# Optimization experiments

Measured on AMD Instinct MI355X. Metric: run time of the kernel, lower is better.

## Reference

```python
import jax, jax.numpy as jnp
import numpy as np

D_MODEL = 1024
NUM_HEADS = 16
HEAD_DIM = D_MODEL // NUM_HEADS
D_FF = 4096
BATCH = 4
SEQ = 2048
LN_EPS = 1e-6
NEG_INF = -1e10


def setup_inputs() -> dict:
    key = jax.random.key(0)
    ks = jax.random.split(key, 8)
    def lin_init(k, fan_in, fan_out):
        # flax default: lecun_normal kernel, zeros bias
        w = jax.random.normal(k, (fan_in, fan_out), jnp.float32) / np.sqrt(fan_in)
        b = jnp.zeros((fan_out,), jnp.float32)
        return w, b
    x = jax.random.normal(ks[0], (BATCH, SEQ, D_MODEL), jnp.float32)
    w_qkv, b_qkv = lin_init(ks[1], D_MODEL, 3 * D_MODEL)
    w_out, b_out = lin_init(ks[2], D_MODEL, D_MODEL)
    w_fc1, b_fc1 = lin_init(ks[3], D_MODEL, D_FF)
    w_fc2, b_fc2 = lin_init(ks[4], D_FF, D_MODEL)
    ln1_scale = jnp.ones((D_MODEL,), jnp.float32)
    ln1_bias = jnp.zeros((D_MODEL,), jnp.float32)
    ln2_scale = jnp.ones((D_MODEL,), jnp.float32)
    ln2_bias = jnp.zeros((D_MODEL,), jnp.float32)
    return {
        'x': x,
        'w_qkv': w_qkv, 'b_qkv': b_qkv,
        'w_out': w_out, 'b_out': b_out,
        'w_fc1': w_fc1, 'b_fc1': b_fc1,
        'w_fc2': w_fc2, 'b_fc2': b_fc2,
        'ln1_scale': ln1_scale, 'ln1_bias': ln1_bias,
        'ln2_scale': ln2_scale, 'ln2_bias': ln2_bias,
    }


def _layernorm(x, scale, bias):
    mu = jnp.mean(x, axis=-1, keepdims=True)
    var = jnp.mean(jnp.square(x - mu), axis=-1, keepdims=True)
    return (x - mu) * jax.lax.rsqrt(var + LN_EPS) * scale + bias


def _attention(x, w_qkv, b_qkv, w_out, b_out):
    B, S, _ = x.shape
    qkv = x @ w_qkv + b_qkv                      # [B,S,3*D]
    qkv = qkv.reshape(B, S, 3, NUM_HEADS, HEAD_DIM)
    q, k, v = qkv[:, :, 0], qkv[:, :, 1], qkv[:, :, 2]   # [B,S,H,D]
    q = q.transpose(0, 2, 1, 3)                  # [B,H,S,D]
    k = k.transpose(0, 2, 1, 3)
    v = v.transpose(0, 2, 1, 3)
    scores = jnp.einsum('bhqd,bhkd->bhqk', q, k) / np.sqrt(HEAD_DIM)
    causal = jnp.tril(jnp.ones((S, S), bool))[None, None]
    scores = jnp.where(causal, scores, NEG_INF)
    attn = jax.nn.softmax(scores, axis=-1)
    out = jnp.einsum('bhqk,bhkd->bhqd', attn, v)  # [B,H,S,D]
    out = out.transpose(0, 2, 1, 3).reshape(B, S, D_MODEL)
    return out @ w_out + b_out


def _mlp(x, w_fc1, b_fc1, w_fc2, b_fc2):
    h = jax.nn.gelu(x @ w_fc1 + b_fc1)  # approximate (tanh) gelu, matching nnx.gelu default
    return h @ w_fc2 + b_fc2


def reference(x, w_qkv, b_qkv, w_out, b_out, w_fc1, b_fc1, w_fc2, b_fc2,
              ln1_scale, ln1_bias, ln2_scale, ln2_bias):
    x = x + _attention(_layernorm(x, ln1_scale, ln1_bias), w_qkv, b_qkv, w_out, b_out)
    x = x + _mlp(_layernorm(x, ln2_scale, ln2_bias), w_fc1, b_fc1, w_fc2, b_fc2)
    return x
```

## Files before the change

kernel.cpp:

```cpp
#include <hip/hip_runtime.h>

typedef unsigned short u16;
typedef unsigned int u32;
typedef __bf16 bf16x8 __attribute__((ext_vector_type(8)));
typedef float f32x4 __attribute__((ext_vector_type(4)));

constexpr int SEQ = 2048;

__device__ __forceinline__ float bf2f(u16 u) {
    u32 x = ((u32)u) << 16;
    return __builtin_bit_cast(float, x);
}
__device__ __forceinline__ u16 f2bf(float f) {
    u32 u = __builtin_bit_cast(u32, f);
    u32 r = u + 0x7fffu + ((u >> 16) & 1u);
    return (u16)(r >> 16);
}
__device__ __forceinline__ u32 cvt_pk_bf16(float a, float b) {
    u32 d;
    asm("v_cvt_pk_bf16_f32 %0, %1, %2" : "=v"(d) : "v"(a), "v"(b));
    return d;
}
__device__ __forceinline__ bf16x8 ld_frag(const u16* p) {
    uint4 u = *(const uint4*)p;
    return __builtin_bit_cast(bf16x8, u);
}
__device__ __forceinline__ float gelu_f(float x) {
    float u = 0.7978845608028654f * (x + 0.044715f * x * x * x);
    float e = exp2f(u * 2.885390081777927f);
    float t = 1.f - 2.f / (1.f + e);
    return 0.5f * x * (1.f + t);
}
__device__ __forceinline__ bool probe_f32(const u32* p) { return (p[0] & 0xFFFFu) == 0u; }

__device__ __forceinline__ void load_lds16(const u16* g, u16* l) {
    __builtin_amdgcn_global_load_lds(
        (const __attribute__((address_space(1))) void*)g,
        (__attribute__((address_space(3))) void*)l, 16, 0, 0);
}

__device__ __forceinline__ void xcd_map(int& bx, int& by) {
    const int gx = gridDim.x;
    const int n = gx * gridDim.y;
    const int orig = blockIdx.y * gx + blockIdx.x;
    const int id = (orig & 7) * (n >> 3) + (orig >> 3);
    bx = id % gx;
    by = id / gx;
}

__global__ __launch_bounds__(256) void convert_to_bf16(const void* __restrict__ in, long long off,
                                                       u16* __restrict__ out, int n,
                                                       const u32* __restrict__ probe) {
    const bool f32 = probe_f32(probe);
    int i = (blockIdx.x * 256 + threadIdx.x) * 4;
    if (i >= n) return;
    if (f32) {
        const float4 v = *(const float4*)((const float*)in + off + i);
        uint2 o;
        o.x = (u32)f2bf(v.x) | ((u32)f2bf(v.y) << 16);
        o.y = (u32)f2bf(v.z) | ((u32)f2bf(v.w) << 16);
        *(uint2*)(out + i) = o;
    } else {
        *(uint2*)(out + i) = *(const uint2*)((const u16*)in + off + i);
    }
}

__global__ __launch_bounds__(256) void transpose_any(const void* __restrict__ in,
                                                     u16* __restrict__ out,
                                                     int K, int N, const u32* __restrict__ probe) {
    const bool f32 = probe_f32(probe);
    __shared__ u16 tile[32][33];
    int tx = threadIdx.x & 31, ty = threadIdx.x >> 5;
    int k0 = blockIdx.y * 32, n0 = blockIdx.x * 32;
    for (int i = 0; i < 32; i += 8) {
        size_t idx = (size_t)(k0 + ty + i) * N + n0 + tx;
        tile[ty + i][tx] = f32 ? f2bf(((const float*)in)[idx]) : ((const u16*)in)[idx];
    }
    __syncthreads();
    for (int i = 0; i < 32; i += 8)
        out[(size_t)(n0 + ty + i) * K + k0 + tx] = tile[tx][ty + i];
}

__global__ __launch_bounds__(256) void fused_cvt_ln(const void* __restrict__ xraw, long long off,
                                                    const u16* __restrict__ sc,
                                                    const u16* __restrict__ bi,
                                                    u16* __restrict__ xbf,
                                                    u16* __restrict__ xn,
                                                    const u32* __restrict__ probe) {
    const bool f32 = probe_f32(probe);
    int row = blockIdx.x;
    int tid = threadIdx.x;
    float v[4];
    if (f32) {
        const float4 q = *(const float4*)((const float*)xraw + off + (size_t)row * 1024 + tid * 4);
        v[0] = q.x; v[1] = q.y; v[2] = q.z; v[3] = q.w;
    } else {
        uint2 u = *(const uint2*)((const u16*)xraw + off + (size_t)row * 1024 + tid * 4);
        v[0] = bf2f((u16)(u.x & 0xffffu)); v[1] = bf2f((u16)(u.x >> 16));
        v[2] = bf2f((u16)(u.y & 0xffffu)); v[3] = bf2f((u16)(u.y >> 16));
    }
    {
        uint2 c;
        c.x = (u32)f2bf(v[0]) | ((u32)f2bf(v[1]) << 16);
        c.y = (u32)f2bf(v[2]) | ((u32)f2bf(v[3]) << 16);
        *(uint2*)(xbf + (size_t)row * 1024 + tid * 4) = c;
    }
    float s1 = 0.f, s2 = 0.f;
    for (int i = 0; i < 4; i++) { s1 += v[i]; s2 += v[i] * v[i]; }
    for (int off2 = 32; off2 >= 1; off2 >>= 1) {
        s1 += __shfl_xor(s1, off2, 64);
        s2 += __shfl_xor(s2, off2, 64);
    }
    __shared__ float red[8];
    int wave = tid >> 6, lane = tid & 63;
    if (lane == 0) { red[wave] = s1; red[4 + wave] = s2; }
    __syncthreads();
    s1 = red[0] + red[1] + red[2] + red[3];
    s2 = red[4] + red[5] + red[6] + red[7];
    float mean = s1 * (1.f / 1024.f);
    float var = s2 * (1.f / 1024.f) - mean * mean;
    float rstd = rsqrtf(var + 1e-6f);
    int c = tid * 4;
    float y0 = (v[0] - mean) * rstd * bf2f(sc[c + 0]) + bf2f(bi[c + 0]);
    float y1 = (v[1] - mean) * rstd * bf2f(sc[c + 1]) + bf2f(bi[c + 1]);
    float y2 = (v[2] - mean) * rstd * bf2f(sc[c + 2]) + bf2f(bi[c + 2]);
    float y3 = (v[3] - mean) * rstd * bf2f(sc[c + 3]) + bf2f(bi[c + 3]);
    uint2 ov;
    ov.x = (u32)f2bf(y0) | ((u32)f2bf(y1) << 16);
    ov.y = (u32)f2bf(y2) | ((u32)f2bf(y3) << 16);
    *(uint2*)(xn + (size_t)row * 1024 + tid * 4) = ov;
}

__global__ __launch_bounds__(256) void layernorm_k(const u16* __restrict__ x,
                                                   const u16* __restrict__ sc,
                                                   const u16* __restrict__ bi,
                                                   u16* __restrict__ out) {
    int row = blockIdx.x;
    int tid = threadIdx.x;
    const u16* xr = x + (size_t)row * 1024;
    uint2 u = *(const uint2*)(xr + tid * 4);
    float v[4];
    v[0] = bf2f((u16)(u.x & 0xffffu));
    v[1] = bf2f((u16)(u.x >> 16));
    v[2] = bf2f((u16)(u.y & 0xffffu));
    v[3] = bf2f((u16)(u.y >> 16));
    float s1 = 0.f, s2 = 0.f;
    for (int i = 0; i < 4; i++) { s1 += v[i]; s2 += v[i] * v[i]; }
    for (int off = 32; off >= 1; off >>= 1) {
        s1 += __shfl_xor(s1, off, 64);
        s2 += __shfl_xor(s2, off, 64);
    }
    __shared__ float red[8];
    int wave = tid >> 6, lane = tid & 63;
    if (lane == 0) { red[wave] = s1; red[4 + wave] = s2; }
    __syncthreads();
    s1 = red[0] + red[1] + red[2] + red[3];
    s2 = red[4] + red[5] + red[6] + red[7];
    float mean = s1 * (1.f / 1024.f);
    float var = s2 * (1.f / 1024.f) - mean * mean;
    float rstd = rsqrtf(var + 1e-6f);
    u32 o0, o1;
    {
        int c = tid * 4;
        float y0 = (v[0] - mean) * rstd * bf2f(sc[c + 0]) + bf2f(bi[c + 0]);
        float y1 = (v[1] - mean) * rstd * bf2f(sc[c + 1]) + bf2f(bi[c + 1]);
        float y2 = (v[2] - mean) * rstd * bf2f(sc[c + 2]) + bf2f(bi[c + 2]);
        float y3 = (v[3] - mean) * rstd * bf2f(sc[c + 3]) + bf2f(bi[c + 3]);
        o0 = (u32)f2bf(y0) | ((u32)f2bf(y1) << 16);
        o1 = (u32)f2bf(y2) | ((u32)f2bf(y3) << 16);
    }
    uint2 ov; ov.x = o0; ov.y = o1;
    *(uint2*)(out + (size_t)row * 1024 + tid * 4) = ov;
}

__device__ __forceinline__ void gemm_core(const u16* __restrict__ A, const u16* __restrict__ Bt,
                                          int K, int bm, int bn,
                                          u16* lA, u16* lB, f32x4 acc[4][4]) {
    const int tid = threadIdx.x, lane = tid & 63, wave = tid >> 6;
    const int wr = (wave >> 1) * 64, wc = (wave & 1) * 64;
    const int g = lane >> 4, l15 = lane & 15;
    const int srow = wave * 32 + (lane >> 3);
    const int gslot = (lane & 7) ^ (lane >> 3);
    const u16* gA = A + (size_t)(bm + srow) * K + gslot * 8;
    const u16* gB = Bt + (size_t)(bn + srow) * K + gslot * 8;
    const int sw = (l15 & 7);
    const int nt = K >> 6;

    {
        u16* dA = lA + wave * 2048;
        u16* dB = lB + wave * 2048;
#pragma unroll
        for (int q = 0; q < 4; q++) {
            load_lds16(gA + q * 8 * K, dA + q * 512);
            load_lds16(gB + q * 8 * K, dB + q * 512);
        }
    }

    for (int t = 0; t < nt; t++) {
        const int cur = (t & 1) * 8192;
        __syncthreads();
        if (t + 1 < nt) {
            const int nxt = ((t + 1) & 1) * 8192;
            const int kk = (t + 1) * 64;
            u16* dA = lA + nxt + wave * 2048;
            u16* dB = lB + nxt + wave * 2048;
#pragma unroll
            for (int q = 0; q < 4; q++) {
                load_lds16(gA + kk + q * 8 * K, dA + q * 512);
                load_lds16(gB + kk + q * 8 * K, dB + q * 512);
            }
        }
        const u16* cA = lA + cur;
        const u16* cB = lB + cur;
#pragma unroll
        for (int kh = 0; kh < 2; kh++) {
            bf16x8 af[4], bfr[4];
#pragma unroll
            for (int i = 0; i < 4; i++)
                af[i] = ld_frag(cA + (wr + i * 16 + l15) * 64 + (((kh * 4 + g) ^ sw) * 8));
#pragma unroll
            for (int j = 0; j < 4; j++)
                bfr[j] = ld_frag(cB + (wc + j * 16 + l15) * 64 + (((kh * 4 + g) ^ sw) * 8));
#pragma unroll
            for (int i = 0; i < 4; i++)
#pragma unroll
                for (int j = 0; j < 4; j++)
                    acc[i][j] = __builtin_amdgcn_mfma_f32_16x16x32_bf16(bfr[j], af[i], acc[i][j], 0, 0, 0);
        }
    }
}

__global__ __launch_bounds__(256) void gemm_bt(const u16* __restrict__ A,
                                               const u16* __restrict__ Bt,
                                               const u16* __restrict__ bias,
                                               const u16* __restrict__ res,
                                               void* __restrict__ out,
                                               int M, int N, int K, int epi,
                                               long long ooff, const u32* __restrict__ probe) {
    __shared__ __align__(16) u16 lA[2 * 128 * 64];
    __shared__ __align__(16) u16 lB[2 * 128 * 64];
    const int tid = threadIdx.x, lane = tid & 63, wave = tid >> 6;
    const int wr = (wave >> 1) * 64, wc = (wave & 1) * 64;
    const int g = lane >> 4, l15 = lane & 15;
    const int bm = blockIdx.y * 128, bn = blockIdx.x * 128;

    f32x4 acc[4][4];
    f32x4 zero = {0.f, 0.f, 0.f, 0.f};
    for (int i = 0; i < 4; i++)
        for (int j = 0; j < 4; j++) acc[i][j] = zero;

    gemm_core(A, Bt, K, bm, bn, lA, lB, acc);

    const bool of32 = (epi == 3) && probe_f32(probe);
    for (int j = 0; j < 4; j++) {
        const int gn0 = bn + wc + j * 16 + g * 4;
        const uint2 bv2 = *(const uint2*)(bias + gn0);
        const float b0 = bf2f((u16)(bv2.x & 0xffffu)), b1 = bf2f((u16)(bv2.x >> 16));
        const float b2 = bf2f((u16)(bv2.y & 0xffffu)), b3 = bf2f((u16)(bv2.y >> 16));
        for (int i = 0; i < 4; i++) {
            const int gm = bm + wr + i * 16 + l15;
            float v0 = acc[i][j][0] + b0, v1 = acc[i][j][1] + b1;
            float v2 = acc[i][j][2] + b2, v3 = acc[i][j][3] + b3;
            if (epi == 1 || epi == 3) {
                const uint2 rv = *(const uint2*)(res + (size_t)gm * N + gn0);
                v0 += bf2f((u16)(rv.x & 0xffffu)); v1 += bf2f((u16)(rv.x >> 16));
                v2 += bf2f((u16)(rv.y & 0xffffu)); v3 += bf2f((u16)(rv.y >> 16));
            } else if (epi == 2) {
                v0 = gelu_f(v0); v1 = gelu_f(v1); v2 = gelu_f(v2); v3 = gelu_f(v3);
            }
            if (epi == 3) {
                if (of32) {
                    float4 o = {v0, v1, v2, v3};
                    *(float4*)((float*)out + ooff + (size_t)gm * N + gn0) = o;
                } else {
                    uint2 o;
                    o.x = cvt_pk_bf16(v0, v1); o.y = cvt_pk_bf16(v2, v3);
                    *(uint2*)((u16*)out + ooff + (size_t)gm * N + gn0) = o;
                }
            } else {
                uint2 o;
                o.x = cvt_pk_bf16(v0, v1); o.y = cvt_pk_bf16(v2, v3);
                *(uint2*)((u16*)out + (size_t)gm * N + gn0) = o;
            }
        }
    }
}

__global__ __launch_bounds__(256) void gemm_qkv(const u16* __restrict__ A,
                                                const u16* __restrict__ Bt,
                                                const u16* __restrict__ bias,
                                                u16* __restrict__ Qg,
                                                u16* __restrict__ Kg,
                                                u16* __restrict__ VTg,
                                                int K) {
    __shared__ __align__(16) u16 lA[2 * 128 * 64];
    __shared__ __align__(16) u16 lB[2 * 128 * 64];
    const int tid = threadIdx.x, lane = tid & 63, wave = tid >> 6;
    const int wr = (wave >> 1) * 64, wc = (wave & 1) * 64;
    const int g = lane >> 4, l15 = lane & 15;
    const int bm = blockIdx.y * 128, bn = blockIdx.x * 128;
    const float QSCALE = 0.18033688011112042f;

    f32x4 acc[4][4];
    f32x4 zero = {0.f, 0.f, 0.f, 0.f};
    for (int i = 0; i < 4; i++)
        for (int j = 0; j < 4; j++) acc[i][j] = zero;

    gemm_core(A, Bt, K, bm, bn, lA, lB, acc);

    for (int j = 0; j < 4; j++) {
        const int gn0 = bn + wc + j * 16 + g * 4;
        const int which = gn0 >> 10;
        const int hh = (gn0 >> 6) & 15, d0 = gn0 & 63;
        const uint2 bv2 = *(const uint2*)(bias + gn0);
        const float b0 = bf2f((u16)(bv2.x & 0xffffu)), b1 = bf2f((u16)(bv2.x >> 16));
        const float b2 = bf2f((u16)(bv2.y & 0xffffu)), b3 = bf2f((u16)(bv2.y >> 16));
        for (int i = 0; i < 4; i++) {
            const int s0 = bm + wr + i * 16 + l15;
            const int b = s0 >> 11, srel = s0 & 2047;
            const int bh = b * 16 + hh;
            const float v0 = acc[i][j][0] + b0, v1 = acc[i][j][1] + b1;
            const float v2 = acc[i][j][2] + b2, v3 = acc[i][j][3] + b3;
            if (which == 0) {
                uint2 o;
                o.x = cvt_pk_bf16(v0 * QSCALE, v1 * QSCALE);
                o.y = cvt_pk_bf16(v2 * QSCALE, v3 * QSCALE);
                *(uint2*)(Qg + ((size_t)bh * SEQ + srel) * 64 + d0) = o;
            } else if (which == 1) {
                uint2 o;
                o.x = cvt_pk_bf16(v0, v1); o.y = cvt_pk_bf16(v2, v3);
                *(uint2*)(Kg + ((size_t)bh * SEQ + srel) * 64 + d0) = o;
            } else {
                VTg[((size_t)bh * 64 + d0 + 0) * SEQ + srel] = f2bf(v0);
                VTg[((size_t)bh * 64 + d0 + 1) * SEQ + srel] = f2bf(v1);
                VTg[((size_t)bh * 64 + d0 + 2) * SEQ + srel] = f2bf(v2);
                VTg[((size_t)bh * 64 + d0 + 3) * SEQ + srel] = f2bf(v3);
            }
        }
    }
}

__device__ __forceinline__ void stage_kv(const u16* Kbh, const u16* Vbh, int kv0,
                                         u16* bK, u16* bV, int lane, int wave) {
    const int r = lane >> 3;
    const int gs = ((lane & 7) ^ r) * 8;
#pragma unroll
    for (int q = 0; q < 2; q++) {
        const int row = q * 32 + wave * 8 + r;
        load_lds16(Kbh + (size_t)(kv0 + row) * 64 + gs, bK + q * 2048 + wave * 512 + lane * 8);
        load_lds16(Vbh + (size_t)row * SEQ + kv0 + gs, bV + q * 2048 + wave * 512 + lane * 8);
    }
}

__global__ __launch_bounds__(256) void flash_attn6(const u16* __restrict__ Qg,
                                                   const u16* __restrict__ Kg,
                                                   const u16* __restrict__ VTg,
                                                   u16* __restrict__ attn) {
    __shared__ __align__(16) u16 lK[2][64 * 64];
    __shared__ __align__(16) u16 lVt[2][64 * 64];
    __shared__ __align__(16) u16 lP[4 * 32 * 72];

    int bxi, byi;
    xcd_map(bxi, byi);
    const int bh = byi;
    const int tid = threadIdx.x, lane = tid & 63, wave = tid >> 6;
    const int g = lane >> 4, l15 = lane & 15;
    const float MASKV = -3.0e4f;

    const u16* Qbh = Qg + (size_t)bh * SEQ * 64;
    const u16* Kbh = Kg + (size_t)bh * SEQ * 64;
    const u16* Vbh = VTg + (size_t)bh * 64 * SEQ;
    u16* myP = lP + wave * 32 * 72;
    const int b = bh >> 4, h = bh & 15;
    const f32x4 zero = {0.f, 0.f, 0.f, 0.f};
    const int sw = (l15 & 7);

    for (int ph = 0; ph < 2; ph++) {
        const int ti = ph ? bxi : (15 - bxi);
        const int q0 = ti * 128;
        const int qw = q0 + wave * 32;
        const int nfull = q0 >> 6;
        const int nt = nfull + 2;

        bf16x8 qf[2][2];
#pragma unroll
        for (int mi = 0; mi < 2; mi++)
#pragma unroll
            for (int kh = 0; kh < 2; kh++)
                qf[mi][kh] = ld_frag(Qbh + (size_t)(qw + mi * 16 + l15) * 64 + kh * 32 + g * 8);

        float l_[2] = {0.f, 0.f};
        f32x4 o[2][4];
        for (int mi = 0; mi < 2; mi++)
            for (int nj = 0; nj < 4; nj++) o[mi][nj] = zero;

        __syncthreads();
        stage_kv(Kbh, Vbh, 0, lK[0], lVt[0], lane, wave);

        for (int t = 0; t < nt; t++) {
            __syncthreads();
            if (t + 1 < nt)
                stage_kv(Kbh, Vbh, (t + 1) * 64, lK[(t + 1) & 1], lVt[(t + 1) & 1], lane, wave);
            const u16* bK = lK[t & 1];
            const u16* bV = lVt[t & 1];
            const bool diag = (t >= nfull);
            const int kv0 = t * 64;

            f32x4 sc[4][2];
#pragma unroll
            for (int ki = 0; ki < 4; ki++)
                for (int mi = 0; mi < 2; mi++) sc[ki][mi] = zero;
#pragma unroll
            for (int kh = 0; kh < 2; kh++) {
                bf16x8 kf[4];
#pragma unroll
                for (int ki = 0; ki < 4; ki++)
                    kf[ki] = ld_frag(bK + (ki * 16 + l15) * 64 + (((kh * 4 + g) ^ sw) * 8));
#pragma unroll
                for (int ki = 0; ki < 4; ki++)
#pragma unroll
                    for (int mi = 0; mi < 2; mi++)
                        sc[ki][mi] = __builtin_amdgcn_mfma_f32_16x16x32_bf16(kf[ki], qf[mi][kh], sc[ki][mi], 0, 0, 0);
            }

#pragma unroll
            for (int mi = 0; mi < 2; mi++) {
                const int qrow = qw + mi * 16 + l15;
                u16* pr = myP + (mi * 16 + l15) * 72 + g * 4;
                float lacc = 0.f;
#pragma unroll
                for (int ki = 0; ki < 4; ki++) {
                    const int kvb = kv0 + ki * 16 + g * 4;
                    float v0 = sc[ki][mi][0], v1 = sc[ki][mi][1];
                    float v2 = sc[ki][mi][2], v3 = sc[ki][mi][3];
                    if (diag) {
                        if (kvb + 0 > qrow) v0 = MASKV;
                        if (kvb + 1 > qrow) v1 = MASKV;
                        if (kvb + 2 > qrow) v2 = MASKV;
                        if (kvb + 3 > qrow) v3 = MASKV;
                    }
                    const float e0 = exp2f(v0), e1 = exp2f(v1);
                    const float e2 = exp2f(v2), e3 = exp2f(v3);
                    lacc += (e0 + e1) + (e2 + e3);
                    uint2 pw;
                    pw.x = cvt_pk_bf16(e0, e1);
                    pw.y = cvt_pk_bf16(e2, e3);
                    *(uint2*)(pr + ki * 16) = pw;
                }
                l_[mi] += lacc;
            }

#pragma unroll
            for (int ks = 0; ks < 2; ks++) {
                bf16x8 pa[2], vb[4];
#pragma unroll
                for (int mi = 0; mi < 2; mi++)
                    pa[mi] = ld_frag(myP + (mi * 16 + l15) * 72 + ks * 32 + g * 8);
#pragma unroll
                for (int nj = 0; nj < 4; nj++)
                    vb[nj] = ld_frag(bV + (nj * 16 + l15) * 64 + (((ks * 4 + g) ^ sw) * 8));
#pragma unroll
                for (int mi = 0; mi < 2; mi++)
#pragma unroll
                    for (int nj = 0; nj < 4; nj++)
                        o[mi][nj] = __builtin_amdgcn_mfma_f32_16x16x32_bf16(pa[mi], vb[nj], o[mi][nj], 0, 0, 0);
            }
        }

#pragma unroll
        for (int mi = 0; mi < 2; mi++) {
            float ls = l_[mi];
            ls += __shfl_xor(ls, 16, 64);
            ls += __shfl_xor(ls, 32, 64);
#pragma unroll
            for (int r = 0; r < 4; r++) {
                const float inv = 1.f / __shfl(ls, g * 4 + r, 64);
                const int row = qw + mi * 16 + g * 4 + r;
                const size_t orow = ((size_t)b * SEQ + row) * 1024 + h * 64;
                for (int nj = 0; nj < 4; nj++)
                    attn[orow + nj * 16 + l15] = f2bf(o[mi][nj][r] * inv);
            }
        }
    }
}

extern "C" void kernel_launch(void* const* d_in, const int* in_sizes, int n_in,
                              void* d_out, int out_size, void* d_ws, size_t ws_size,
                              hipStream_t stream) {
    const u32* probe = (const u32*)d_in[9];
    char* ws = (char*)d_ws;
    const size_t MB = 1048576;
    auto T = [&](size_t mb) { return (u16*)(ws + mb * MB); };
    auto conv = [&](const void* src, long long off, u16* dst, int n) {
        convert_to_bf16<<<(n / 4 + 255) / 256, 256, 0, stream>>>(src, off, dst, n, probe);
    };

    if (ws_size >= 160 * MB) {
        u16* xn1 = T(0), *Qg = T(16), *Kg = T(32), *VTg = T(48), *hbuf = T(0);
        u16* attn = T(64), *xn2 = T(64), *xbf = T(80), *resid1 = T(96);
        u16* wTq = T(128), *wTo = T(134), *wT1 = T(136), *wT2 = T(144), *vecs = T(152);
        u16 *bqkvC = vecs, *boutC = vecs + 3072, *bfc1C = vecs + 4096, *bfc2C = vecs + 8192;
        u16 *ln1sC = vecs + 9216, *ln1bC = vecs + 10240, *ln2sC = vecs + 11264, *ln2bC = vecs + 12288;
        conv(d_in[2], 0, bqkvC, 3072); conv(d_in[4], 0, boutC, 1024);
        conv(d_in[6], 0, bfc1C, 4096); conv(d_in[8], 0, bfc2C, 1024);
        conv(d_in[9], 0, ln1sC, 1024); conv(d_in[10], 0, ln1bC, 1024);
        conv(d_in[11], 0, ln2sC, 1024); conv(d_in[12], 0, ln2bC, 1024);
        transpose_any<<<dim3(96, 32), 256, 0, stream>>>(d_in[1], wTq, 1024, 3072, probe);
        transpose_any<<<dim3(32, 32), 256, 0, stream>>>(d_in[3], wTo, 1024, 1024, probe);
        transpose_any<<<dim3(128, 32), 256, 0, stream>>>(d_in[5], wT1, 1024, 4096, probe);
        transpose_any<<<dim3(32, 128), 256, 0, stream>>>(d_in[7], wT2, 4096, 1024, probe);
        fused_cvt_ln<<<8192, 256, 0, stream>>>(d_in[0], 0, ln1sC, ln1bC, xbf, xn1, probe);
        gemm_qkv<<<dim3(24, 64), 256, 0, stream>>>(xn1, wTq, bqkvC, Qg, Kg, VTg, 1024);
        flash_attn6<<<dim3(8, 64), 256, 0, stream>>>(Qg, Kg, VTg, attn);
        gemm_bt<<<dim3(8, 64), 256, 0, stream>>>(attn, wTo, boutC, xbf, resid1, 8192, 1024, 1024, 1, 0, probe);
        layernorm_k<<<8192, 256, 0, stream>>>(resid1, ln2sC, ln2bC, xn2);
        gemm_bt<<<dim3(32, 64), 256, 0, stream>>>(xn2, wT1, bfc1C, nullptr, hbuf, 8192, 4096, 1024, 2, 0, probe);
        gemm_bt<<<dim3(8, 64), 256, 0, stream>>>(hbuf, wT2, bfc2C, resid1, d_out, 8192, 1024, 4096, 3, 0, probe);
    } else {
        u16* vecs = T(0);
        u16 *bqkvC = vecs, *boutC = vecs + 3072, *bfc1C = vecs + 4096, *bfc2C = vecs + 8192;
        u16 *ln1sC = vecs + 9216, *ln1bC = vecs + 10240, *ln2sC = vecs + 11264, *ln2bC = vecs + 12288;
        u16* wTq = T(1), *wTo = T(7), *wT1 = T(9), *wT2 = T(17);
        u16* xbf = T(25), *xn = T(29), *Qg = T(33), *Kg = T(37), *VTg = T(41);
        u16* attn_b = T(45), *resid_b = T(49), *h_b = T(53);
        conv(d_in[2], 0, bqkvC, 3072); conv(d_in[4], 0, boutC, 1024);
        conv(d_in[6], 0, bfc1C, 4096); conv(d_in[8], 0, bfc2C, 1024);
        conv(d_in[9], 0, ln1sC, 1024); conv(d_in[10], 0, ln1bC, 1024);
        conv(d_in[11], 0, ln2sC, 1024); conv(d_in[12], 0, ln2bC, 1024);
        transpose_any<<<dim3(96, 32), 256, 0, stream>>>(d_in[1], wTq, 1024, 3072, probe);
        transpose_any<<<dim3(32, 32), 256, 0, stream>>>(d_in[3], wTo, 1024, 1024, probe);
        transpose_any<<<dim3(128, 32), 256, 0, stream>>>(d_in[5], wT1, 1024, 4096, probe);
        transpose_any<<<dim3(32, 128), 256, 0, stream>>>(d_in[7], wT2, 4096, 1024, probe);
        for (int b = 0; b < 4; b++) {
            const long long ro = (long long)b * 2048 * 1024;
            fused_cvt_ln<<<2048, 256, 0, stream>>>(d_in[0], ro, ln1sC, ln1bC, xbf, xn, probe);
            gemm_qkv<<<dim3(24, 16), 256, 0, stream>>>(xn, wTq, bqkvC, Qg, Kg, VTg, 1024);
            flash_attn6<<<dim3(8, 16), 256, 0, stream>>>(Qg, Kg, VTg, attn_b);
            gemm_bt<<<dim3(8, 16), 256, 0, stream>>>(attn_b, wTo, boutC, xbf, resid_b, 2048, 1024, 1024, 1, 0, probe);
            layernorm_k<<<2048, 256, 0, stream>>>(resid_b, ln2sC, ln2bC, xn);
            for (int c = 0; c < 2; c++) {
                u16* xnc = xn + (size_t)c * 1024 * 1024;
                u16* resc = resid_b + (size_t)c * 1024 * 1024;
                gemm_bt<<<dim3(32, 8), 256, 0, stream>>>(xnc, wT1, bfc1C, nullptr, h_b, 1024, 4096, 1024, 2, 0, probe);
                gemm_bt<<<dim3(8, 8), 256, 0, stream>>>(h_b, wT2, bfc2C, resc, d_out, 1024, 1024, 4096, 3, ro + (long long)c * 1048576, probe);
            }
        }
    }
}
```

Before: 553.8 us.

## Add 256x256-tile 8-wave GEMM for FC1 and single-buffer the 128 GEMMs

Adds a 512-thread GEMM kernel with 256x256 output tiles, double-buffered LDS staging with explicit vmcnt waits and barriers, and MFMA priority hints, and uses it for the FC1+GELU projection. The larger tile raises operand reuse per LDS load and cuts global traffic. Separately, the existing 128x128 gemm_core used by QKV, out-proj and FC2 drops from double to single-buffered LDS with two barriers per k-step. That frees shared memory for occupancy but removes load/compute overlap in those GEMMs.

```diff
diff --git a/kernel.cpp b/kernel.cpp
--- a/kernel.cpp
+++ b/kernel.cpp
@@ -183,49 +183,109 @@
     const int gslot = (lane & 7) ^ (lane >> 3);
     const u16* gA = A + (size_t)(bm + srow) * K + gslot * 8;
     const u16* gB = Bt + (size_t)(bn + srow) * K + gslot * 8;
+    u16* lAb = lA + wave * 2048;
+    u16* lBb = lB + wave * 2048;
+    const int sw = (l15 & 7);
+
+    for (int kk = 0; kk < K; kk += 64) {
+        __syncthreads();
+#pragma unroll
+        for (int q = 0; q < 4; q++) {
+            load_lds16(gA + kk + q * 8 * K, lAb + q * 512);
+            load_lds16(gB + kk + q * 8 * K, lBb + q * 512);
+        }
+        __syncthreads();
+#pragma unroll
+        for (int kh = 0; kh < 2; kh++) {
+            bf16x8 af[4], bfr[4];
+#pragma unroll
+            for (int i = 0; i < 4; i++)
+                af[i] = ld_frag(lA + (wr + i * 16 + l15) * 64 + (((kh * 4 + g) ^ sw) * 8));
+#pragma unroll
+            for (int j = 0; j < 4; j++)
+                bfr[j] = ld_frag(lB + (wc + j * 16 + l15) * 64 + (((kh * 4 + g) ^ sw) * 8));
+#pragma unroll
+            for (int i = 0; i < 4; i++)
+#pragma unroll
+                for (int j = 0; j < 4; j++)
+                    acc[i][j] = __builtin_amdgcn_mfma_f32_16x16x32_bf16(bfr[j], af[i], acc[i][j], 0, 0, 0);
+        }
+    }
+}
+
+__device__ __forceinline__ void gemm256_core(const u16* __restrict__ A, const u16* __restrict__ Bt,
+                                             int K, int bm, int bn,
+                                             u16* lA, u16* lB, f32x4 acc[8][4]) {
+    const int tid = threadIdx.x, lane = tid & 63, wave = tid >> 6;
+    const int wr = (wave >> 2) * 128, wc = (wave & 3) * 64;
+    const int g = lane >> 4, l15 = lane & 15;
+    const int srow = wave * 32 + (lane >> 3);
+    const int gslot = (lane & 7) ^ (lane >> 3);
+    const u16* gA = A + (size_t)(bm + srow) * K + gslot * 8;
+    const u16* gB = Bt + (size_t)(bn + srow) * K + gslot * 8;
     const int sw = (l15 & 7);
     const int nt = K >> 6;
 
-    {
-        u16* dA = lA + wave * 2048;
-        u16* dB = lB + wave * 2048;
+    auto STAGE = [&](int t) {
+        const int c = (t & 1) * 16384;
+        const int kk = t * 64;
+        u16* dA = lA + c + wave * 2048;
+        u16* dB = lB + c + wave * 2048;
 #pragma unroll
         for (int q = 0; q < 4; q++) {
-            load_lds16(gA + q * 8 * K, dA + q * 512);
-            load_lds16(gB + q * 8 * K, dB + q * 512);
-        }
-    }
+            load_lds16(gA + kk + q * 8 * K, dA + q * 512);
+            load_lds16(gB + kk + q * 8 * K, dB + q * 512);
+        }
+    };
+
+    STAGE(0);
+    STAGE(1);
+    asm volatile("s_waitcnt vmcnt(8)" ::: "memory");
+    __builtin_amdgcn_sched_barrier(0);
+    __builtin_amdgcn_s_barrier();
+    __builtin_amdgcn_sched_barrier(0);
 
     for (int t = 0; t < nt; t++) {
-        const int cur = (t & 1) * 8192;
-        __syncthreads();
+        const u16* cA = lA + (t & 1) * 16384;
+        const u16* cB = lB + (t & 1) * 16384;
+        bf16x8 bfr[2][4];
+#pragma unroll
+        for (int kh = 0; kh < 2; kh++)
+#pragma unroll
+            for (int j = 0; j < 4; j++)
+                bfr[kh][j] = ld_frag(cB + (wc + j * 16 + l15) * 64 + (((kh * 4 + g) ^ sw) * 8));
+#pragma unroll
+        for (int half = 0; half < 2; half++) {
+#pragma unroll
+            for (int kh = 0; kh < 2; kh++) {
+                bf16x8 af[4];
+#pragma unroll
+                for (int i = 0; i < 4; i++)
+                    af[i] = ld_frag(cA + (wr + (half * 4 + i) * 16 + l15) * 64 + (((kh * 4 + g) ^ sw) * 8));
+                __builtin_amdgcn_s_setprio(1);
+#pragma unroll
+                for (int i = 0; i < 4; i++)
+#pragma unroll
+                    for (int j = 0; j < 4; j++)
+                        acc[half * 4 + i][j] =
+                            __builtin_amdgcn_mfma_f32_16x16x32_bf16(bfr[kh][j], af[i], acc[half * 4 + i][j], 0, 0, 0);
+                __builtin_amdgcn_s_setprio(0);
+            }
+        }
         if (t + 1 < nt) {
-            const int nxt = ((t + 1) & 1) * 8192;
-            const int kk = (t + 1) * 64;
-            u16* dA = lA + nxt + wave * 2048;
-            u16* dB = lB + nxt + wave * 2048;
-#pragma unroll
-            for (int q = 0; q < 4; q++) {
-                load_lds16(gA + kk + q * 8 * K, dA + q * 512);
-                load_lds16(gB + kk + q * 8 * K, dB + q * 512);
-            }
-        }
-        const u16* cA = lA + cur;
-        const u16* cB = lB + cur;
-#pragma unroll
-        for (int kh = 0; kh < 2; kh++) {
-            bf16x8 af[4], bfr[4];
-#pragma unroll
-            for (int i = 0; i < 4; i++)
-                af[i] = ld_frag(cA + (wr + i * 16 + l15) * 64 + (((kh * 4 + g) ^ sw) * 8));
-#pragma unroll
-            for (int j = 0; j < 4; j++)
-                bfr[j] = ld_frag(cB + (wc + j * 16 + l15) * 64 + (((kh * 4 + g) ^ sw) * 8));
-#pragma unroll
-            for (int i = 0; i < 4; i++)
-#pragma unroll
-                for (int j = 0; j < 4; j++)
-                    acc[i][j] = __builtin_amdgcn_mfma_f32_16x16x32_bf16(bfr[j], af[i], acc[i][j], 0, 0, 0);
+            asm volatile("s_waitcnt lgkmcnt(0)" ::: "memory");
+            __builtin_amdgcn_sched_barrier(0);
+            __builtin_amdgcn_s_barrier();
+            __builtin_amdgcn_sched_barrier(0);
+            if (t + 2 < nt) {
+                STAGE(t + 2);
+                asm volatile("s_waitcnt vmcnt(8)" ::: "memory");
+            } else {
+                asm volatile("s_waitcnt vmcnt(0)" ::: "memory");
+            }
+            __builtin_amdgcn_sched_barrier(0);
+            __builtin_amdgcn_s_barrier();
+            __builtin_amdgcn_sched_barrier(0);
         }
     }
 }
@@ -237,8 +297,8 @@
                                                void* __restrict__ out,
                                                int M, int N, int K, int epi,
                                                long long ooff, const u32* __restrict__ probe) {
-    __shared__ __align__(16) u16 lA[2 * 128 * 64];
-    __shared__ __align__(16) u16 lB[2 * 128 * 64];
+    __shared__ __align__(16) u16 lA[128 * 64];
+    __shared__ __align__(16) u16 lB[128 * 64];
     const int tid = threadIdx.x, lane = tid & 63, wave = tid >> 6;
     const int wr = (wave >> 1) * 64, wc = (wave & 1) * 64;
     const int g = lane >> 4, l15 = lane & 15;
@@ -286,6 +346,49 @@
     }
 }
 
+__global__ __launch_bounds__(512, 2) void gemm_bt256(const u16* __restrict__ A,
+                                                     const u16* __restrict__ Bt,
+                                                     const u16* __restrict__ bias,
+                                                     const u16* __restrict__ res,
+                                                     u16* __restrict__ out,
+                                                     int M, int N, int K, int epi) {
+    __shared__ __align__(16) u16 lA[2 * 256 * 64];
+    __shared__ __align__(16) u16 lB[2 * 256 * 64];
+    const int tid = threadIdx.x, lane = tid & 63, wave = tid >> 6;
+    const int wr = (wave >> 2) * 128, wc = (wave & 3) * 64;
+    const int g = lane >> 4, l15 = lane & 15;
+    const int bm = blockIdx.y * 256, bn = blockIdx.x * 256;
+
+    f32x4 acc[8][4];
+    f32x4 zero = {0.f, 0.f, 0.f, 0.f};
+    for (int i = 0; i < 8; i++)
+        for (int j = 0; j < 4; j++) acc[i][j] = zero;
+
+    gemm256_core(A, Bt, K, bm, bn, lA, lB, acc);
+
+    for (int j = 0; j < 4; j++) {
+        const int gn0 = bn + wc + j * 16 + g * 4;
+        const uint2 bv2 = *(const uint2*)(bias + gn0);
+        const float b0 = bf2f((u16)(bv2.x & 0xffffu)), b1 = bf2f((u16)(bv2.x >> 16));
+        const float b2 = bf2f((u16)(bv2.y & 0xffffu)), b3 = bf2f((u16)(bv2.y >> 16));
+        for (int i = 0; i < 8; i++) {
+            const int gm = bm + wr + i * 16 + l15;
+            float v0 = acc[i][j][0] + b0, v1 = acc[i][j][1] + b1;
+            float v2 = acc[i][j][2] + b2, v3 = acc[i][j][3] + b3;
+            if (epi == 1) {
+                const uint2 rv = *(const uint2*)(res + (size_t)gm * N + gn0);
+                v0 += bf2f((u16)(rv.x & 0xffffu)); v1 += bf2f((u16)(rv.x >> 16));
+                v2 += bf2f((u16)(rv.y & 0xffffu)); v3 += bf2f((u16)(rv.y >> 16));
+            } else if (epi == 2) {
+                v0 = gelu_f(v0); v1 = gelu_f(v1); v2 = gelu_f(v2); v3 = gelu_f(v3);
+            }
+            uint2 o;
+            o.x = cvt_pk_bf16(v0, v1); o.y = cvt_pk_bf16(v2, v3);
+            *(uint2*)(out + (size_t)gm * N + gn0) = o;
+        }
+    }
+}
+
 __global__ __launch_bounds__(256) void gemm_qkv(const u16* __restrict__ A,
                                                 const u16* __restrict__ Bt,
                                                 const u16* __restrict__ bias,
@@ -293,8 +396,8 @@
                                                 u16* __restrict__ Kg,
                                                 u16* __restrict__ VTg,
                                                 int K) {
-    __shared__ __align__(16) u16 lA[2 * 128 * 64];
-    __shared__ __align__(16) u16 lB[2 * 128 * 64];
+    __shared__ __align__(16) u16 lA[128 * 64];
+    __shared__ __align__(16) u16 lB[128 * 64];
     const int tid = threadIdx.x, lane = tid & 63, wave = tid >> 6;
     const int wr = (wave >> 1) * 64, wc = (wave & 1) * 64;
     const int g = lane >> 4, l15 = lane & 15;
@@ -514,7 +617,7 @@
         flash_attn6<<<dim3(8, 64), 256, 0, stream>>>(Qg, Kg, VTg, attn);
         gemm_bt<<<dim3(8, 64), 256, 0, stream>>>(attn, wTo, boutC, xbf, resid1, 8192, 1024, 1024, 1, 0, probe);
         layernorm_k<<<8192, 256, 0, stream>>>(resid1, ln2sC, ln2bC, xn2);
-        gemm_bt<<<dim3(32, 64), 256, 0, stream>>>(xn2, wT1, bfc1C, nullptr, hbuf, 8192, 4096, 1024, 2, 0, probe);
+        gemm_bt256<<<dim3(16, 32), 512, 0, stream>>>(xn2, wT1, bfc1C, nullptr, hbuf, 8192, 4096, 1024, 2);
         gemm_bt<<<dim3(8, 64), 256, 0, stream>>>(hbuf, wT2, bfc2C, resid1, d_out, 8192, 1024, 4096, 3, 0, probe);
     } else {
         u16* vecs = T(0);
```

New measurement: 650.9 us. 1.18x slower.
